# Optimization experiments

Measured on AMD Instinct MI355X. Metric: run time of the kernel, lower is better.

The kernel has to match this reference:

```python
import jax, jax.numpy as jnp
import numpy as np


def _shift(x, k):
    # roll time axis forward by k, zero-filling the first k steps
    if k == 0:
        return x
    return jnp.pad(x, ((0, 0), (k, 0), (0, 0)))[:, : x.shape[1]]


def _stu_conv(u, v, n):
    # u: (B,L,D), v: (L,K) spectral filters; non-tensordot branch of conv()
    B, L, D = u.shape
    K = v.shape[1]
    sgn = jnp.where(jnp.arange(L) % 2 == 1, -1.0, 1.0).astype(jnp.float32)[None, :, None, None]
    ue = jnp.broadcast_to(u[:, :, None, :], (B, L, K, D)).astype(jnp.float32)
    U = jnp.stack([ue, ue * sgn], axis=-1)                     # (B,L,K,D,2)
    Uf = jnp.fft.rfft(U, n=n, axis=1)
    vf = jnp.fft.rfft(v.astype(jnp.float32)[None, :, :, None, None], n=n, axis=1)
    Uc = jnp.fft.irfft(vf * Uf, n=n, axis=1)[:, :L]            # (B,L,K,D,2)
    U_plus = Uc[..., 0]
    U_minus = Uc[..., 1] * sgn
    return U_plus.astype(u.dtype), U_minus.astype(u.dtype)


def setup_inputs() -> dict:
    key = jax.random.key(0)
    ks = jax.random.split(key, 6)
    B, L, D, K, k_u, k_y = 2, 1024, 512, 16, 3, 2
    u = jax.random.normal(ks[0], (B, L, D), jnp.float32)
    filters = jax.random.normal(ks[1], (L, K), jnp.float32) / np.float32(np.sqrt(L))
    M_u = jax.random.normal(ks[2], (D, k_u, D), jnp.float32) * 0.01
    M_y = jax.random.normal(ks[3], (D, k_y, D), jnp.float32) * 0.01
    M_phi_plus = jax.random.normal(ks[4], (K, D, D), jnp.float32) * 0.01
    M_phi_minus = jax.random.normal(ks[5], (K, D, D), jnp.float32) * 0.01
    return {"u": u, "filters": filters, "M_u": M_u, "M_y": M_y,
            "M_phi_plus": M_phi_plus, "M_phi_minus": M_phi_minus}


def reference(u, filters, M_u, M_y, M_phi_plus, M_phi_minus):
    B, L, D = u.shape
    n = 1 << int(np.ceil(np.log2(2 * L - 1)))  # nearest power of two >= 2L-1
    k_u = M_u.shape[1]
    k_y = M_y.shape[1]

    # FFT-based long convolution with the +/- sign trick
    U_plus, U_minus = _stu_conv(u, filters, n)
    spectral = (jnp.einsum('blkd,kdo->blo', U_plus, M_phi_plus)
                + jnp.einsum('blkd,kdo->blo', U_minus, M_phi_minus))

    # input-AR term of compute_ar_strict: sum_j u[t+1-j] @ M_u[:, j-1].T (shifts 0..k_u-1)
    u_sh = jnp.stack([_shift(u, j - 1) for j in range(1, k_u + 1)], axis=1)  # (B,k_u,L,D)
    y_in = jnp.einsum('bjlf,ijf->bli', u_sh, M_u)

    z = spectral + y_in  # (B,L,D)

    # output-AR recurrence of compute_ar_strict as a scan
    def step(y_buf, z_t):
        y_t = z_t + jnp.einsum('bjf,djf->bd', y_buf, M_y)
        y_buf = jnp.concatenate([y_t[:, None], y_buf[:, :-1]], axis=1)
        return y_buf, y_t

    _, ys = jax.lax.scan(step, jnp.zeros((B, k_y, D), z.dtype), jnp.swapaxes(z, 0, 1))
    return jnp.swapaxes(ys, 0, 1)  # (B,L,D)
```

## Files before the change

kernel.cpp:

```cpp
#include <hip/hip_runtime.h>
#include <hip/hip_bf16.h>


using bf16 = __hip_bfloat16;
typedef __attribute__((ext_vector_type(8))) short bf16x8;
typedef __attribute__((ext_vector_type(4))) float f32x4;

#define B_   2
#define L_   1024
#define D_   512
#define K_   16
#define KT   17920
#define ROWS 2048
#define NTAP 6
#define PBLD 3584
#define SPLITD 14
#define SPLITR 6
#define ZBROWS 1032

#define WAIT_VM4 0x0F74
#define WAIT_VM0 0x0F70

__device__ __forceinline__ void gll16(const void* g, void* l) {
    __builtin_amdgcn_global_load_lds(
        (const __attribute__((address_space(1))) unsigned int*)g,
        (__attribute__((address_space(3))) unsigned int*)l, 16, 0, 0);
}

__global__ void prep_all(const float* __restrict__ u, const float* __restrict__ fil,
                         const float* __restrict__ Mu, const float* __restrict__ My,
                         const float* __restrict__ Mp, const float* __restrict__ Mm,
                         bf16* __restrict__ U, bf16* __restrict__ BT,
                         bf16* __restrict__ PB, bf16* __restrict__ W,
                         bf16* __restrict__ Myb, bf16* __restrict__ BTT,
                         bf16* __restrict__ uPT) {
    __shared__ bf16 t[64][72];
    int bid = blockIdx.x, tid = threadIdx.x;
    auto pack4 = [](float4 v) {
        ushort4 o; bf16 h;
        h = __float2bfloat16(v.x); o.x = *(unsigned short*)&h;
        h = __float2bfloat16(v.y); o.y = *(unsigned short*)&h;
        h = __float2bfloat16(v.z); o.z = *(unsigned short*)&h;
        h = __float2bfloat16(v.w); o.w = *(unsigned short*)&h;
        return o;
    };
    if (bid < 3072) {
        int e4 = bid * 256 + tid;
        int r = e4 / 384, rem = e4 % 384;
        int tt = rem >> 7, f = (rem & 127) * 4;
        int b = r >> 10, l = r & 1023;
        float4 v = {0.f, 0.f, 0.f, 0.f};
        if (l >= tt) v = *(const float4*)&u[((size_t)b * L_ + l - tt) * D_ + f];
        *(ushort4*)&U[(size_t)r * KT + 16384 + tt * 512 + f] = pack4(v);
    } else if (bid < 3840) {
        int e4 = (bid - 3072) * 256 + tid;
        int o = e4 / 384, tf4 = (e4 % 384) * 4;
        float4 v = *(const float4*)&Mu[(size_t)o * 1536 + tf4];
        *(ushort4*)&BT[(size_t)o * KT + 16384 + tf4] = pack4(v);
    } else if (bid < 4352) {
        int e4 = (bid - 3840) * 256 + tid;
        int n = e4 >> 8, c4 = (e4 & 255) * 4;
        float4 v;
        if (c4 < 512) {
            v.x = (n == c4) ? 1.f : 0.f;     v.y = (n == c4 + 1) ? 1.f : 0.f;
            v.z = (n == c4 + 2) ? 1.f : 0.f; v.w = (n == c4 + 3) ? 1.f : 0.f;
        } else v = *(const float4*)&My[(size_t)n * 1024 + (c4 - 512)];
        *(ushort4*)&PB[(size_t)n * PBLD + c4] = pack4(v);
    } else if (bid < 5120) {
        int tile = bid - 4352;
        int set = tile >> 8, rem = tile & 255;
        int k = rem >> 4, g = (rem >> 2) & 3, kb = rem & 3;
        for (int idx = tid; idx < 4096; idx += 256) {
            int i = idx >> 5, jp = idx & 31;
            int j = ((jp >> 3) ^ ((i >> 1) & 3)) * 8 + (jp & 7);
            int x = g * 128 + i - kb * 32 - j - (set == 2 ? 1 : 0);
            float v = 0.f;
            if (x >= 0) {
                int row = (set == 0) ? 2 * x : 2 * x + 1;
                v = fil[row * K_ + k];
            }
            W[(size_t)tile * 4096 + idx] = __float2bfloat16(v);
        }
    } else if (bid < 5632) {
        int e4 = (bid - 5120) * 256 + tid;
        float4 v = *(const float4*)&My[(size_t)e4 * 4];
        *(ushort4*)&Myb[(size_t)e4 * 4] = pack4(v);
    } else {
        int tt = bid - 5632;
        int zb = tt >> 6, rem = tt & 63;
        int bx = rem & 7, by = rem >> 3;
        int col = tid & 63, r0 = (tid >> 6) * 16;
        if (zb < 32) {
            int dt = bx * 64, ot = by * 64, c = zb;
            int k = c & 15;
            const float* sp = Mp + (size_t)k * D_ * D_;
            const float* sm = Mm + (size_t)k * D_ * D_;
            float sg = (c < 16) ? 1.f : -1.f;
            for (int i = 0; i < 16; ++i) {
                size_t o_ = (size_t)(dt + r0 + i) * D_ + ot + col;
                t[r0 + i][col] = __float2bfloat16(sp[o_] + sg * sm[o_]);
            }
            __syncthreads();
            for (int i = 0; i < 16; ++i)
                BT[(size_t)(ot + r0 + i) * KT + c * D_ + dt + col] = t[col][r0 + i];
        } else if (zb < 34) {
            int h = zb - 32;
            int dt = bx * 64, ft = by * 64;
            for (int i = 0; i < 16; ++i)
                t[r0 + i][col] = __float2bfloat16(My[(size_t)(dt + r0 + i) * 1024 + (1 - h) * 512 + ft + col]);
            __syncthreads();
            for (int i = 0; i < 16; ++i)
                BTT[(size_t)(ft + r0 + i) * 1024 + h * 512 + dt + col] = t[col][r0 + i];
        } else {
            for (int it = 0; it < 4; ++it) {
                int b = it >> 1, p = it & 1;
                int mt = bx * 64, dt = by * 64;
                __syncthreads();
                for (int i = 0; i < 16; ++i)
                    t[r0 + i][col] = __float2bfloat16(u[((size_t)b * L_ + 2 * (mt + r0 + i) + p) * D_ + dt + col]);
                __syncthreads();
                for (int i = 0; i < 16; ++i)
                    uPT[((size_t)it * 512 + dt + r0 + i) * 512 + mt + col] = t[col][r0 + i];
            }
        }
    }
}

__device__ __forceinline__ void phi_body(
    const bf16* A, int lda, const bf16* BT, int ldb,
    bf16* out, int ldo, int klen, const bf16* add, int lad,
    int row0, int col0, bf16* sA, bf16* sB)
{
    const int tid = threadIdx.x, lane = tid & 63, wave = tid >> 6;
    const int wm = (wave & 1) * 64, wn = (wave >> 1) * 64;
    const int ml = lane & 15, q = lane >> 4;
    const int srow = lane >> 2, scol = (((lane & 3) ^ ((srow >> 1) & 3))) * 8;
    const int swz = ((ml >> 1) & 3);
    f32x4 acc[4][4] = {};

    for (int k = 0; k < klen; k += 32) {
        __syncthreads();
        #pragma unroll
        for (int repi = 0; repi < 2; ++repi) {
            int a = wave + repi * 4;
            gll16(A  + (size_t)(row0 + a * 16 + srow) * lda + k + scol, &sA[a * 512]);
            gll16(BT + (size_t)(col0 + a * 16 + srow) * ldb + k + scol, &sB[a * 512]);
        }
        __syncthreads();
        bf16x8 af[4], bfr[4];
        #pragma unroll
        for (int i = 0; i < 4; ++i)
            af[i] = *(const bf16x8*)&sA[(wm + i * 16 + ml) * 32 + (q ^ swz) * 8];
        #pragma unroll
        for (int j = 0; j < 4; ++j)
            bfr[j] = *(const bf16x8*)&sB[(wn + j * 16 + ml) * 32 + (q ^ swz) * 8];
        #pragma unroll
        for (int i = 0; i < 4; ++i)
            #pragma unroll
            for (int j = 0; j < 4; ++j)
                acc[i][j] = __builtin_amdgcn_mfma_f32_16x16x32_bf16(af[i], bfr[j], acc[i][j], 0, 0, 0);
    }
    #pragma unroll
    for (int i = 0; i < 4; ++i)
        #pragma unroll
        for (int j = 0; j < 4; ++j)
            #pragma unroll
            for (int reg = 0; reg < 4; ++reg) {
                int r = row0 + wm + i * 16 + q * 4 + reg;
                int cc = col0 + wn + j * 16 + ml;
                float v = acc[i][j][reg];
                if (add) v += __bfloat162float(add[(size_t)r * lad + cc]);
                out[(size_t)r * ldo + cc] = __float2bfloat16(v);
            }
}

__global__ void k_ztaps(const bf16* __restrict__ partD, float* __restrict__ z,
                        bf16* __restrict__ zbuf, bf16* PB, const bf16* BTT) {
    __shared__ bf16 sA[4096];
    __shared__ bf16 sB[4096];
    int bid = blockIdx.x;
    if (bid < 32) {
        int row0 = (bid & 3) * 128, col0 = (bid >> 2) * 128;
        phi_body(PB + 3 * 512, PBLD, BTT, 1024, PB + 5 * 512, PBLD, 1024,
                 nullptr, 0, row0, col0, sA, sB);
        return;
    }
    if (bid == 32) {
        ushort4 z4 = {0, 0, 0, 0};
        for (int i = 0; i < 8; ++i) {
            int e4 = i * 256 + threadIdx.x;
            int b = e4 >> 10, rem = e4 & 1023;
            int g = rem >> 7, c4 = (rem & 127) * 4;
            *(ushort4*)&zbuf[(size_t)(b * ZBROWS + g) * 512 + c4] = z4;
        }
        return;
    }
    int t = (bid - 33) * 256 + threadIdx.x;
    int r = t >> 7, f4 = (t & 127) * 4;
    const ushort4* p = (const ushort4*)partD;
    float4 s = {0.f, 0.f, 0.f, 0.f};
    #pragma unroll
    for (int c = 0; c < SPLITD; ++c) {
        ushort4 v = p[(size_t)c * (ROWS * D_ / 4) + t];
        s.x += __uint_as_float((unsigned)v.x << 16);
        s.y += __uint_as_float((unsigned)v.y << 16);
        s.z += __uint_as_float((unsigned)v.z << 16);
        s.w += __uint_as_float((unsigned)v.w << 16);
    }
    ((float4*)z)[t] = s;
    ushort4 zb4;
    { bf16 h;
      h = __float2bfloat16(s.x); zb4.x = *(unsigned short*)&h;
      h = __float2bfloat16(s.y); zb4.y = *(unsigned short*)&h;
      h = __float2bfloat16(s.z); zb4.z = *(unsigned short*)&h;
      h = __float2bfloat16(s.w); zb4.w = *(unsigned short*)&h; }
    int b = r >> 10, li = r & 1023;
    *(ushort4*)&zbuf[(size_t)(b * ZBROWS + 8 + li) * 512 + f4] = zb4;
}

__global__ void reduce_out(const float* __restrict__ z, const bf16* __restrict__ partR,
                           float* __restrict__ out) {
    int t = blockIdx.x * 256 + threadIdx.x;
    if (t >= ROWS * D_ / 4) return;
    float4 s = ((const float4*)z)[t];
    const ushort4* p = (const ushort4*)partR;
    #pragma unroll
    for (int c = 0; c < SPLITR; ++c) {
        ushort4 v = p[(size_t)c * (ROWS * D_ / 4) + t];
        s.x += __uint_as_float((unsigned)v.x << 16);
        s.y += __uint_as_float((unsigned)v.y << 16);
        s.z += __uint_as_float((unsigned)v.z << 16);
        s.w += __uint_as_float((unsigned)v.w << 16);
    }
    ((float4*)out)[t] = s;
}

__global__ __launch_bounds__(256, 3) void conv_misc(
    const bf16* __restrict__ W, const bf16* __restrict__ uPT,
    bf16* __restrict__ U,
    const bf16* PB, const bf16* BTT, const bf16* Myb)
{
    __shared__ bf16 sA[3][4096];
    __shared__ bf16 sB[3][4096];
    const int z = blockIdx.z;
    if (z < 3) {
        int row0 = blockIdx.x * 128, col0 = blockIdx.y * 128;
        bf16* BTTw = (bf16*)BTT; bf16* PBw = (bf16*)PB;
        if (z == 0)
            phi_body(PB, PBLD, BTT, 1024, PBw + 2 * 512, PBLD, 1024,
                     nullptr, 0, row0, col0, &sA[0][0], &sB[0][0]);
        else if (z == 1)
            phi_body(BTT + 512, 1024, Myb + 512, 1024,
                     BTTw + (size_t)512 * 1024, 1024, 512,
                     nullptr, 0, row0, col0, &sA[0][0], &sB[0][0]);
        else
            phi_body(BTT + 512, 1024, Myb, 1024,
                     BTTw + (size_t)512 * 1024 + 512, 1024, 512,
                     BTT, 1024, row0, col0, &sA[0][0], &sB[0][0]);
        return;
    }
    const int zc = z - 3;
    const int mt = 3 - blockIdx.x, dt = blockIdx.y * 128;
    const int t = zc & 3, b = (zc >> 2) & 1, k = zc >> 3;
    const int pb_ = t & 1;
    const int p = (t & 1) ^ (t >> 1);
    const int set = (t < 2) ? 0 : (t == 2 ? 1 : 2);
    const int ch = (t < 2) ? k : 16 + k;
    const int plane = b * 2 + pb_;
    const int tid = threadIdx.x, lane = tid & 63, wave = tid >> 6;
    const int wm = (wave & 1) * 64, wn = (wave >> 1) * 64;
    const int ml = lane & 15, q = lane >> 4;
    const int srow = lane >> 2, scol = (((lane & 3) ^ ((srow >> 1) & 3))) * 8;
    const int swz = ((ml >> 1) & 3);
    f32x4 acc[4][4] = {};
    const int n = (mt + 1) * 4;

    const bf16* bB0 = uPT + ((size_t)plane * 512 + dt + wave * 16       + srow) * 512 + scol;
    const bf16* bB1 = uPT + ((size_t)plane * 512 + dt + (wave + 4) * 16 + srow) * 512 + scol;
    const bf16* wbase = W + ((size_t)(set * 16 + k) * 16) * 4096;
    auto stage = [&](int s, int buf) {
        const bf16* wt = wbase + ((size_t)((mt - (s >> 2)) * 4 + (s & 3))) * 4096;
        gll16(wt + wave * 512 + lane * 8, &sA[buf][wave * 512]);
        gll16(wt + (wave + 4) * 512 + lane * 8, &sA[buf][(wave + 4) * 512]);
        gll16(bB0 + s * 32, &sB[buf][wave * 512]);
        gll16(bB1 + s * 32, &sB[buf][(wave + 4) * 512]);
    };
    auto compute = [&](int c) {
        bf16x8 af[4], bfr[4];
        #pragma unroll
        for (int i = 0; i < 4; ++i)
            af[i] = *(const bf16x8*)&sA[c][(wm + i * 16 + ml) * 32 + (q ^ swz) * 8];
        #pragma unroll
        for (int j = 0; j < 4; ++j)
            bfr[j] = *(const bf16x8*)&sB[c][(wn + j * 16 + ml) * 32 + (q ^ swz) * 8];
        #pragma unroll
        for (int i = 0; i < 4; ++i)
            #pragma unroll
            for (int j = 0; j < 4; ++j)
                acc[i][j] = __builtin_amdgcn_mfma_f32_16x16x32_bf16(af[i], bfr[j], acc[i][j], 0, 0, 0);
    };
    stage(0, 0); stage(1, 1);
    int c = 0, nb = 2;
    for (int i = 0; i < n - 1; ++i) {
        __builtin_amdgcn_s_waitcnt(WAIT_VM4);
        __builtin_amdgcn_s_barrier();
        if (i + 2 < n) stage(i + 2, nb);
        compute(c);
        c = (c == 2) ? 0 : c + 1; nb = (nb == 2) ? 0 : nb + 1;
    }
    __builtin_amdgcn_s_waitcnt(WAIT_VM0);
    __builtin_amdgcn_s_barrier();
    compute(c);

    #pragma unroll
    for (int i = 0; i < 4; ++i)
        #pragma unroll
        for (int j = 0; j < 4; ++j)
            #pragma unroll
            for (int reg = 0; reg < 4; ++reg) {
                int m = mt * 128 + wm + i * 16 + q * 4 + reg;
                int l = 2 * m + p;
                int d = dt + wn + j * 16 + ml;
                U[(size_t)(b * L_ + l) * KT + ch * 512 + d] = __float2bfloat16(acc[i][j][reg]);
            }
}

__global__ __launch_bounds__(512, 1) void gemm_d(
    const bf16* __restrict__ U, const bf16* __restrict__ BT,
    bf16* __restrict__ part, const bf16* PB, const bf16* BTT)
{
    __shared__ bf16 sA[3][8192];
    __shared__ bf16 sB[3][8192];
    int id = blockIdx.x;
    const int tid = threadIdx.x, lane = tid & 63, wave = tid >> 6;
    if (id < 32) {
        if (wave >= 4) {
            for (int i = 0; i < 64; ++i) __syncthreads();
            return;
        }
        int r0_ = (id & 3) * 128, c0_ = (id >> 2) * 128;
        phi_body(PB + 512, PBLD, BTT, 1024, (bf16*)PB + 3 * 512, PBLD, 1024,
                 nullptr, 0, r0_, c0_, &sA[0][0], &sB[0][0]);
        return;
    }
    id -= 32;
    const int zz = id >> 4;
    const int n_ = id & 15;
    const int row0 = (n_ >> 1) * 256, col0 = (n_ & 1) * 256;
    const int kc = KT / SPLITD;
    const int k0 = zz * kc;
    const int n = kc >> 5;

    const int wm = (wave & 3) * 64, wn = (wave >> 2) * 128;
    const int ml = lane & 15, q = lane >> 4;
    const int srow = lane >> 2, scol = (((lane & 3) ^ ((srow >> 1) & 3))) * 8;
    const int swz = ((ml >> 1) & 3);
    f32x4 acc[4][8] = {};

    const int a0 = 2 * wave, a1 = 2 * wave + 1;
    const bf16* bA0 = U  + (size_t)(row0 + a0 * 16 + srow) * KT + k0 + scol;
    const bf16* bA1 = U  + (size_t)(row0 + a1 * 16 + srow) * KT + k0 + scol;
    const bf16* bB0 = BT + (size_t)(col0 + a0 * 16 + srow) * KT + k0 + scol;
    const bf16* bB1 = BT + (size_t)(col0 + a1 * 16 + srow) * KT + k0 + scol;
    auto stage = [&](int s, int buf) {
        gll16(bA0 + s * 32, &sA[buf][a0 * 512]);
        gll16(bA1 + s * 32, &sA[buf][a1 * 512]);
        gll16(bB0 + s * 32, &sB[buf][a0 * 512]);
        gll16(bB1 + s * 32, &sB[buf][a1 * 512]);
    };
    auto compute = [&](int c) {
        bf16x8 af[4], bfr[8];
        #pragma unroll
        for (int i = 0; i < 4; ++i)
            af[i] = *(const bf16x8*)&sA[c][(wm + i * 16 + ml) * 32 + (q ^ swz) * 8];
        #pragma unroll
        for (int j = 0; j < 8; ++j)
            bfr[j] = *(const bf16x8*)&sB[c][(wn + j * 16 + ml) * 32 + (q ^ swz) * 8];
        #pragma unroll
        for (int i = 0; i < 4; ++i)
            #pragma unroll
            for (int j = 0; j < 8; ++j)
                acc[i][j] = __builtin_amdgcn_mfma_f32_16x16x32_bf16(af[i], bfr[j], acc[i][j], 0, 0, 0);
    };
    stage(0, 0); stage(1, 1);
    int c = 0, nb = 2;
    for (int i = 0; i < n - 1; ++i) {
        __builtin_amdgcn_s_waitcnt(WAIT_VM4);
        __builtin_amdgcn_s_barrier();
        if (i + 2 < n) stage(i + 2, nb);
        compute(c);
        c = (c == 2) ? 0 : c + 1; nb = (nb == 2) ? 0 : nb + 1;
    }
    __builtin_amdgcn_s_waitcnt(WAIT_VM0);
    __builtin_amdgcn_s_barrier();
    compute(c);

    bf16* o = part + (size_t)zz * ROWS * D_;
    #pragma unroll
    for (int i = 0; i < 4; ++i)
        #pragma unroll
        for (int j = 0; j < 8; ++j)
            #pragma unroll
            for (int reg = 0; reg < 4; ++reg) {
                int r = row0 + wm + i * 16 + q * 4 + reg;
                int cc = col0 + wn + j * 16 + ml;
                o[(size_t)r * D_ + cc] = __float2bfloat16(acc[i][j][reg]);
            }
}

__device__ __forceinline__ void mm128_pair(
    const bf16* Abase, int alda, const bf16* Bbase, int ldb, int n,
    bf16* o, int row0, int col0, bf16 (*sA)[4096], bf16 (*sB)[4096])
{
    const int tid = threadIdx.x, lane = tid & 63, wave = tid >> 6;
    const int wm = (wave & 1) * 64, wn = (wave >> 1) * 64;
    const int ml = lane & 15, q = lane >> 4;
    const int srow = lane >> 2, scol = (((lane & 3) ^ ((srow >> 1) & 3))) * 8;
    const int swz = ((ml >> 1) & 3);
    f32x4 acc[4][4] = {};

    const bf16* bA0 = Abase + (size_t)(wave * 16 + srow) * alda + scol;
    const bf16* bA1 = Abase + (size_t)((wave + 4) * 16 + srow) * alda + scol;
    const bf16* bB0 = Bbase + (size_t)(wave * 16 + srow) * ldb + scol;
    const bf16* bB1 = Bbase + (size_t)((wave + 4) * 16 + srow) * ldb + scol;
    auto stage = [&](int s) {
        int buf = s & 3;
        gll16(bA0 + s * 32, &sA[buf][wave * 512]);
        gll16(bA1 + s * 32, &sA[buf][(wave + 4) * 512]);
        gll16(bB0 + s * 32, &sB[buf][wave * 512]);
        gll16(bB1 + s * 32, &sB[buf][(wave + 4) * 512]);
    };
    auto compute = [&](int c) {
        bf16x8 af[4], bfr[4];
        #pragma unroll
        for (int i = 0; i < 4; ++i)
            af[i] = *(const bf16x8*)&sA[c][(wm + i * 16 + ml) * 32 + (q ^ swz) * 8];
        #pragma unroll
        for (int j = 0; j < 4; ++j)
            bfr[j] = *(const bf16x8*)&sB[c][(wn + j * 16 + ml) * 32 + (q ^ swz) * 8];
        #pragma unroll
        for (int i = 0; i < 4; ++i)
            #pragma unroll
            for (int j = 0; j < 4; ++j)
                acc[i][j] = __builtin_amdgcn_mfma_f32_16x16x32_bf16(af[i], bfr[j], acc[i][j], 0, 0, 0);
    };
    stage(0); stage(1);
    const int npair = n >> 1;
    for (int p = 0; p < npair; ++p) {
        __builtin_amdgcn_s_waitcnt(WAIT_VM0);
        __builtin_amdgcn_s_barrier();
        if (2 * p + 2 < n) { stage(2 * p + 2); stage(2 * p + 3); }
        compute((2 * p) & 3);
        compute((2 * p + 1) & 3);
    }
    #pragma unroll
    for (int i = 0; i < 4; ++i)
        #pragma unroll
        for (int j = 0; j < 4; ++j)
            #pragma unroll
            for (int reg = 0; reg < 4; ++reg) {
                int r = row0 + wm + i * 16 + q * 4 + reg;
                int cc = col0 + wn + j * 16 + ml;
                o[(size_t)r * D_ + cc] = __float2bfloat16(acc[i][j][reg]);
            }
}

__global__ __launch_bounds__(256, 2) void gemm_r(
    const bf16* __restrict__ zbuf, const bf16* __restrict__ BT,
    bf16* __restrict__ part)
{
    __shared__ bf16 sA[4][4096];
    __shared__ bf16 sB[4][4096];
    const int row0 = blockIdx.x * 128, col0 = blockIdx.y * 128;
    const int zz = blockIdx.z;
    const int s = 1 + zz;
    const int b = row0 >> 10, li0 = row0 & 1023;
    mm128_pair(zbuf + ((size_t)(b * ZBROWS + 8 + li0 - s)) * 512, 512,
               BT + (size_t)col0 * PBLD + (size_t)zz * 512, PBLD,
               16, part + (size_t)zz * ROWS * D_, row0, col0, sA, sB);
}

extern "C" void kernel_launch(void* const* d_in, const int* in_sizes, int n_in,
                              void* d_out, int out_size, void* d_ws, size_t ws_size,
                              hipStream_t stream) {
    const float* u   = (const float*)d_in[0];
    const float* fil = (const float*)d_in[1];
    const float* Mu  = (const float*)d_in[2];
    const float* My  = (const float*)d_in[3];
    const float* Mp  = (const float*)d_in[4];
    const float* Mm  = (const float*)d_in[5];
    float* out = (float*)d_out;

    char* ws = (char*)d_ws;
    size_t off = 0;
    auto alloc = [&](size_t bytes) { void* p = ws + off; off = (off + bytes + 255) & ~(size_t)255; return p; };
    bf16*  U    = (bf16*) alloc((size_t)ROWS * KT * 2);
    bf16*  BT   = (bf16*) alloc((size_t)512 * KT * 2);
    bf16*  PB   = (bf16*) alloc((size_t)512 * PBLD * 2);
    bf16*  BTT  = (bf16*) alloc((size_t)1024 * 1024 * 2);
    bf16*  Myb  = (bf16*) alloc((size_t)512 * 1024 * 2);
    float* z    = (float*)alloc((size_t)ROWS * D_ * 4);
    bf16*  zb   = (bf16*) alloc((size_t)B_ * ZBROWS * 512 * 2);
    char*  region = (char*)alloc((size_t)16 * ROWS * D_ * 2);
    bf16*  W    = (bf16*)region;
    bf16*  uPT  = (bf16*)(region + (size_t)768 * 4096 * 2);
    bf16*  partD = (bf16*)region;
    bf16*  partR = (bf16*)region;

    prep_all<<<7872, 256, 0, stream>>>(u, fil, Mu, My, Mp, Mm,
                                       U, BT, PB, W, Myb, BTT, uPT);

    conv_misc<<<dim3(4, 4, 131), 256, 0, stream>>>(W, uPT, U, PB, BTT, Myb);

    gemm_d<<<256, 512, 0, stream>>>(U, BT, partD, PB, BTT);

    k_ztaps<<<1057, 256, 0, stream>>>(partD, z, zb, PB, BTT);

    gemm_r<<<dim3(16, 4, SPLITR), 256, 0, stream>>>(zb, PB + 512, partR);

    reduce_out<<<(ROWS * D_ / 4 + 255) / 256, 256, 0, stream>>>(z, partR, out);
}
```

Measured before the change: 244.9 us.

## Triple-buffer phi GEMM body and deepen gemm_d prefetch to four stages

The helper GEMM used for the phi/AR matrix products is turned from a single-buffered loop with two __syncthreads per k-step into a three-stage async global-to-LDS pipeline with one barrier per step. It is meant to hide load latency behind MFMA work. The main split-K gemm_d kernel moves from three to four LDS buffers, with prefetch distance three and a matching vmcnt wait. The idle waves' barrier count is adjusted to match the new barrier count. LDS use grows, to 128KB in gemm_d and 48KB in k_ztaps, which could limit occupancy for the kernels that share these blocks.

```diff
diff --git a/kernel.cpp b/kernel.cpp
--- a/kernel.cpp
+++ b/kernel.cpp
@@ -18,6 +18,7 @@
 #define SPLITR 6
 #define ZBROWS 1032
 
+#define WAIT_VM8 0x0F78
 #define WAIT_VM4 0x0F74
 #define WAIT_VM0 0x0F70
 
@@ -126,10 +127,10 @@
     }
 }
 
-__device__ __forceinline__ void phi_body(
+__device__ __forceinline__ void phi_pipe(
     const bf16* A, int lda, const bf16* BT, int ldb,
     bf16* out, int ldo, int klen, const bf16* add, int lad,
-    int row0, int col0, bf16* sA, bf16* sB)
+    int row0, int col0, bf16* sAb, bf16* sBb)
 {
     const int tid = threadIdx.x, lane = tid & 63, wave = tid >> 6;
     const int wm = (wave & 1) * 64, wn = (wave >> 1) * 64;
@@ -137,29 +138,44 @@
     const int srow = lane >> 2, scol = (((lane & 3) ^ ((srow >> 1) & 3))) * 8;
     const int swz = ((ml >> 1) & 3);
     f32x4 acc[4][4] = {};
-
-    for (int k = 0; k < klen; k += 32) {
-        __syncthreads();
+    const int n = klen >> 5;
+
+    auto stg = [&](int s) {
+        int buf = s % 3;
         #pragma unroll
         for (int repi = 0; repi < 2; ++repi) {
             int a = wave + repi * 4;
-            gll16(A  + (size_t)(row0 + a * 16 + srow) * lda + k + scol, &sA[a * 512]);
-            gll16(BT + (size_t)(col0 + a * 16 + srow) * ldb + k + scol, &sB[a * 512]);
+            gll16(A  + (size_t)(row0 + a * 16 + srow) * lda + s * 32 + scol,
+                  &sAb[buf * 4096 + a * 512]);
+            gll16(BT + (size_t)(col0 + a * 16 + srow) * ldb + s * 32 + scol,
+                  &sBb[buf * 4096 + a * 512]);
         }
-        __syncthreads();
+    };
+    auto cmp = [&](int c) {
         bf16x8 af[4], bfr[4];
         #pragma unroll
         for (int i = 0; i < 4; ++i)
-            af[i] = *(const bf16x8*)&sA[(wm + i * 16 + ml) * 32 + (q ^ swz) * 8];
+            af[i] = *(const bf16x8*)&sAb[c * 4096 + (wm + i * 16 + ml) * 32 + (q ^ swz) * 8];
         #pragma unroll
         for (int j = 0; j < 4; ++j)
-            bfr[j] = *(const bf16x8*)&sB[(wn + j * 16 + ml) * 32 + (q ^ swz) * 8];
+            bfr[j] = *(const bf16x8*)&sBb[c * 4096 + (wn + j * 16 + ml) * 32 + (q ^ swz) * 8];
         #pragma unroll
         for (int i = 0; i < 4; ++i)
             #pragma unroll
             for (int j = 0; j < 4; ++j)
                 acc[i][j] = __builtin_amdgcn_mfma_f32_16x16x32_bf16(af[i], bfr[j], acc[i][j], 0, 0, 0);
-    }
+    };
+    stg(0); stg(1);
+    for (int i = 0; i < n - 1; ++i) {
+        __builtin_amdgcn_s_waitcnt(WAIT_VM4);
+        __builtin_amdgcn_s_barrier();
+        if (i + 2 < n) stg(i + 2);
+        cmp(i % 3);
+    }
+    __builtin_amdgcn_s_waitcnt(WAIT_VM0);
+    __builtin_amdgcn_s_barrier();
+    cmp((n - 1) % 3);
+
     #pragma unroll
     for (int i = 0; i < 4; ++i)
         #pragma unroll
@@ -176,12 +192,12 @@
 
 __global__ void k_ztaps(const bf16* __restrict__ partD, float* __restrict__ z,
                         bf16* __restrict__ zbuf, bf16* PB, const bf16* BTT) {
-    __shared__ bf16 sA[4096];
-    __shared__ bf16 sB[4096];
+    __shared__ bf16 sA[3 * 4096];
+    __shared__ bf16 sB[3 * 4096];
     int bid = blockIdx.x;
     if (bid < 32) {
         int row0 = (bid & 3) * 128, col0 = (bid >> 2) * 128;
-        phi_body(PB + 3 * 512, PBLD, BTT, 1024, PB + 5 * 512, PBLD, 1024,
+        phi_pipe(PB + 3 * 512, PBLD, BTT, 1024, PB + 5 * 512, PBLD, 1024,
                  nullptr, 0, row0, col0, sA, sB);
         return;
     }
@@ -247,14 +263,14 @@
         int row0 = blockIdx.x * 128, col0 = blockIdx.y * 128;
         bf16* BTTw = (bf16*)BTT; bf16* PBw = (bf16*)PB;
         if (z == 0)
-            phi_body(PB, PBLD, BTT, 1024, PBw + 2 * 512, PBLD, 1024,
+            phi_pipe(PB, PBLD, BTT, 1024, PBw + 2 * 512, PBLD, 1024,
                      nullptr, 0, row0, col0, &sA[0][0], &sB[0][0]);
         else if (z == 1)
-            phi_body(BTT + 512, 1024, Myb + 512, 1024,
+            phi_pipe(BTT + 512, 1024, Myb + 512, 1024,
                      BTTw + (size_t)512 * 1024, 1024, 512,
                      nullptr, 0, row0, col0, &sA[0][0], &sB[0][0]);
         else
-            phi_body(BTT + 512, 1024, Myb, 1024,
+            phi_pipe(BTT + 512, 1024, Myb, 1024,
                      BTTw + (size_t)512 * 1024 + 512, 1024, 512,
                      BTT, 1024, row0, col0, &sA[0][0], &sB[0][0]);
         return;
@@ -329,17 +345,17 @@
     const bf16* __restrict__ U, const bf16* __restrict__ BT,
     bf16* __restrict__ part, const bf16* PB, const bf16* BTT)
 {
-    __shared__ bf16 sA[3][8192];
-    __shared__ bf16 sB[3][8192];
+    __shared__ bf16 sA[4][8192];
+    __shared__ bf16 sB[4][8192];
     int id = blockIdx.x;
     const int tid = threadIdx.x, lane = tid & 63, wave = tid >> 6;
     if (id < 32) {
         if (wave >= 4) {
-            for (int i = 0; i < 64; ++i) __syncthreads();
+            for (int i = 0; i < 32; ++i) __builtin_amdgcn_s_barrier();
             return;
         }
         int r0_ = (id & 3) * 128, c0_ = (id >> 2) * 128;
-        phi_body(PB + 512, PBLD, BTT, 1024, (bf16*)PB + 3 * 512, PBLD, 1024,
+        phi_pipe(PB + 512, PBLD, BTT, 1024, (bf16*)PB + 3 * 512, PBLD, 1024,
                  nullptr, 0, r0_, c0_, &sA[0][0], &sB[0][0]);
         return;
     }
@@ -362,7 +378,8 @@
     const bf16* bA1 = U  + (size_t)(row0 + a1 * 16 + srow) * KT + k0 + scol;
     const bf16* bB0 = BT + (size_t)(col0 + a0 * 16 + srow) * KT + k0 + scol;
     const bf16* bB1 = BT + (size_t)(col0 + a1 * 16 + srow) * KT + k0 + scol;
-    auto stage = [&](int s, int buf) {
+    auto stage = [&](int s) {
+        int buf = s & 3;
         gll16(bA0 + s * 32, &sA[buf][a0 * 512]);
         gll16(bA1 + s * 32, &sA[buf][a1 * 512]);
         gll16(bB0 + s * 32, &sB[buf][a0 * 512]);
@@ -382,18 +399,19 @@
             for (int j = 0; j < 8; ++j)
                 acc[i][j] = __builtin_amdgcn_mfma_f32_16x16x32_bf16(af[i], bfr[j], acc[i][j], 0, 0, 0);
     };
-    stage(0, 0); stage(1, 1);
-    int c = 0, nb = 2;
-    for (int i = 0; i < n - 1; ++i) {
-        __builtin_amdgcn_s_waitcnt(WAIT_VM4);
+    stage(0); stage(1); stage(2);
+    for (int i = 0; i <= n - 3; ++i) {
+        __builtin_amdgcn_s_waitcnt(WAIT_VM8);
         __builtin_amdgcn_s_barrier();
-        if (i + 2 < n) stage(i + 2, nb);
-        compute(c);
-        c = (c == 2) ? 0 : c + 1; nb = (nb == 2) ? 0 : nb + 1;
-    }
+        if (i + 3 < n) stage(i + 3);
+        compute(i & 3);
+    }
+    __builtin_amdgcn_s_waitcnt(WAIT_VM4);
+    __builtin_amdgcn_s_barrier();
+    compute((n - 2) & 3);
     __builtin_amdgcn_s_waitcnt(WAIT_VM0);
     __builtin_amdgcn_s_barrier();
-    compute(c);
+    compute((n - 1) & 3);
 
     bf16* o = part + (size_t)zz * ROWS * D_;
     #pragma unroll
```

Measured after the change: 251.5 us. 1.03x slower.
